# Optimization experiments

Hardware: AMD Instinct MI355X
Metric: run time of the kernel (lower is better)

Reference implementation:

```python
import jax, jax.numpy as jnp
import numpy as np

B, T, D = 4, 2048, 1024

def layer_norm(x, gamma, bias):
    # NOTE: faithfully reproduces the source's (buggy) LN: x - mu/sqrt(var), unbiased var
    mu = jnp.mean(x, axis=-1, keepdims=True)
    var = jnp.var(x, axis=-1, ddof=1, keepdims=True)
    return (x - mu / jnp.sqrt(var)) * gamma + bias

def setup_inputs() -> dict:
    key = jax.random.key(0)
    ks = jax.random.split(key, 8)
    scale = 1.0 / np.sqrt(D)
    return {
        'x': jax.random.normal(ks[0], (B, T, D), dtype=jnp.float32),
        'gamma1': jnp.ones((D,), jnp.float32),
        'beta1': jnp.zeros((D,), jnp.float32),
        'w_q': jax.random.uniform(ks[1], (D, D), jnp.float32, -scale, scale),
        'w_k': jax.random.uniform(ks[2], (D, D), jnp.float32, -scale, scale),
        'w_v': jax.random.uniform(ks[3], (D, D), jnp.float32, -scale, scale),
        'gamma2': jnp.ones((D,), jnp.float32),
        'beta2': jnp.zeros((D,), jnp.float32),
        'W1': jax.random.uniform(ks[4], (D, D), jnp.float32, -scale, scale),
        'b1': jnp.zeros((D,), jnp.float32),
        'W2': jax.random.uniform(ks[5], (D, D), jnp.float32, -scale, scale),
        'b2': jnp.zeros((D,), jnp.float32),
    }

def reference(x, gamma1, beta1, w_q, w_k, w_v, gamma2, beta2, W1, b1, W2, b2):
    d_model = x.shape[-1]
    t = x.shape[1]
    h = layer_norm(x, gamma1, beta1)
    q = jnp.einsum('btk,kd->btd', h, w_q)
    k = jnp.einsum('btk,kd->btd', h, w_k)
    v = jnp.einsum('btk,kd->btd', h, w_v)
    scale = 1.0 / jnp.sqrt(jnp.asarray(d_model, x.dtype))
    causal = jnp.tril(jnp.ones((t, t), dtype=bool))
    mask = jnp.where(causal, 0.0, -jnp.inf).astype(x.dtype)
    scores = jnp.einsum('bqd,bkd->bqk', q, k) * scale + mask
    attn = jax.nn.softmax(scores, axis=-1)
    y = jnp.einsum('bqt,btd->bqd', attn, v) + x
    h2 = layer_norm(y, gamma2, beta2)
    out = jnp.maximum(h2 @ W1 + b1, 0.0) @ W2 + b2
    return out + y
```

## Files before the change

### kernel.cpp

```cpp
#include <hip/hip_runtime.h>
#include <hip/hip_bf16.h>
#include <math.h>

using bf16 = __hip_bfloat16;

static constexpr int Bn = 4;
static constexpr int Tn = 2048;
static constexpr int Dn = 1024;

typedef __attribute__((ext_vector_type(8))) short bf16x8;
typedef __attribute__((ext_vector_type(4))) float f32x4;

__device__ __forceinline__ float ldf(float v) { return v; }
__device__ __forceinline__ float ldf(bf16 v) { return __bfloat162float(v); }
__device__ __forceinline__ bf16 f2b(float v) { return __float2bfloat16(v); }
__device__ __forceinline__ float b2f(short s) {
    return __uint_as_float(((unsigned)(unsigned short)s) << 16);
}
__device__ __forceinline__ short f2bs(float v) {
    bf16 t = __float2bfloat16(v);
    return *reinterpret_cast<short*>(&t);
}

template <typename T> __device__ __forceinline__ T from_float(float v);
template <> __device__ __forceinline__ float from_float<float>(float v) { return v; }
template <> __device__ __forceinline__ bf16 from_float<bf16>(float v) { return f2b(v); }

__device__ __forceinline__ void load4(const float* p, float* v) {
    const float4 t = *(const float4*)p;
    v[0] = t.x; v[1] = t.y; v[2] = t.z; v[3] = t.w;
}
__device__ __forceinline__ void load4(const bf16* p, float* v) {
    const short4 t = *(const short4*)p;
    v[0] = b2f(t.x); v[1] = b2f(t.y); v[2] = b2f(t.z); v[3] = b2f(t.w);
}

__device__ __forceinline__ void async_copy16(const bf16* g, bf16* l) {
    __builtin_amdgcn_global_load_lds(
        (const __attribute__((address_space(1))) void*)g,
        (__attribute__((address_space(3))) void*)l,
        16, 0, 0);
}

template <int BN, int EPI, typename OutT, bool RELU>
__global__ __launch_bounds__(512, 2) void gemm8p(
    const bf16* __restrict__ A, const bf16* __restrict__ Bm,
    OutT* __restrict__ C, const float* __restrict__ bias,
    const bf16* __restrict__ res, bf16* __restrict__ vtp,
    int K, int lda, int ldb, int ldc)
{
    static_assert(EPI != 1 || BN == 128, "V-transpose epilogue needs BN=128");
    constexpr int BM = 256, BK = 32;
    constexpr int NT = BN / 64;
    constexpr int BUFE = (BM + BN) * BK;
    __shared__ __align__(16) bf16 smem[3 * BUFE];

    const int bm = blockIdx.x, bn = blockIdx.y;
    const int tid = threadIdx.x;
    const int wave = tid >> 6;
    const int lane = tid & 63;
    const int wm = wave >> 2;
    const int wn = wave & 3;
    const int lr = lane >> 2;
    const int lc = (lane & 3) * 8;
    const int arow = lane & 15;
    const int kq = (lane >> 4) * 8;

    const int NK = K / BK;

    const bf16* gA0 = A + (size_t)(bm * BM + wave * 16 + lr) * lda + lc;
    const bf16* gA1 = A + (size_t)(bm * BM + (wave + 8) * 16 + lr) * lda + lc;
    const bf16* gB0 = Bm + (size_t)(bn * BN + wave * 16 + lr) * ldb + lc;
    const bf16* gB1 = (BN == 256)
        ? Bm + (size_t)(bn * BN + (wave + 8) * 16 + lr) * ldb + lc : nullptr;

    f32x4 acc[8][NT] = {};

    {
        bf16* As0 = smem;
        bf16* Bs0 = smem + BM * BK;
        bf16* As1 = smem + BUFE;
        bf16* Bs1 = smem + BUFE + BM * BK;
        async_copy16(gA0, As0 + wave * 512);
        async_copy16(gA1, As0 + (wave + 8) * 512);
        async_copy16(gB0, Bs0 + wave * 512);
        if constexpr (BN == 256) async_copy16(gB1, Bs0 + (wave + 8) * 512);
        async_copy16(gA0 + BK, As1 + wave * 512);
        async_copy16(gA1 + BK, As1 + (wave + 8) * 512);
        async_copy16(gB0 + BK, Bs1 + wave * 512);
        if constexpr (BN == 256) async_copy16(gB1 + BK, Bs1 + (wave + 8) * 512);
    }
    if constexpr (BN == 256) asm volatile("s_waitcnt vmcnt(4)" ::: "memory");
    else                     asm volatile("s_waitcnt vmcnt(3)" ::: "memory");
    __builtin_amdgcn_s_barrier();

    int cb = 0;
    int sb = 2;
    for (int kt = 0; kt < NK; ++kt) {
        const bf16* As = smem + cb * BUFE;
        const bf16* Bs = As + BM * BK;
        const bool st = (kt + 2) < NK;
        const int koff = (kt + 2) * BK;

        bf16x8 af[8], bf0[NT / 2];
#pragma unroll
        for (int mt = 0; mt < 8; ++mt)
            af[mt] = *(const bf16x8*)&As[(wm * 8 + mt) * 512 + arow * 32 + kq];
#pragma unroll
        for (int nt = 0; nt < NT / 2; ++nt)
            bf0[nt] = *(const bf16x8*)&Bs[(wn * NT + nt) * 512 + arow * 32 + kq];
        if (st) {
            bf16* Ad = smem + sb * BUFE;
            async_copy16(gA0 + koff, Ad + wave * 512);
            async_copy16(gA1 + koff, Ad + (wave + 8) * 512);
        }
        __builtin_amdgcn_s_barrier();
        asm volatile("s_waitcnt lgkmcnt(0)" ::: "memory");
        __builtin_amdgcn_sched_barrier(0);
        __builtin_amdgcn_s_setprio(1);
#pragma unroll
        for (int mt = 0; mt < 8; ++mt)
#pragma unroll
            for (int nt = 0; nt < NT / 2; ++nt)
                acc[mt][nt] = __builtin_amdgcn_mfma_f32_16x16x32_bf16(
                    af[mt], bf0[nt], acc[mt][nt], 0, 0, 0);
        __builtin_amdgcn_s_setprio(0);
        __builtin_amdgcn_s_barrier();

        bf16x8 bf1[NT / 2];
#pragma unroll
        for (int nt = 0; nt < NT / 2; ++nt)
            bf1[nt] = *(const bf16x8*)&Bs[(wn * NT + NT / 2 + nt) * 512 + arow * 32 + kq];
        if (st) {
            bf16* Bd = smem + sb * BUFE + BM * BK;
            async_copy16(gB0 + koff, Bd + wave * 512);
            if constexpr (BN == 256) async_copy16(gB1 + koff, Bd + (wave + 8) * 512);
        }
        __builtin_amdgcn_s_barrier();
        asm volatile("s_waitcnt lgkmcnt(0)" ::: "memory");
        __builtin_amdgcn_sched_barrier(0);
        __builtin_amdgcn_s_setprio(1);
#pragma unroll
        for (int mt = 0; mt < 8; ++mt)
#pragma unroll
            for (int nt = 0; nt < NT / 2; ++nt)
                acc[mt][NT / 2 + nt] = __builtin_amdgcn_mfma_f32_16x16x32_bf16(
                    af[mt], bf1[nt], acc[mt][NT / 2 + nt], 0, 0, 0);
        __builtin_amdgcn_s_setprio(0);
        if (st) {
            if constexpr (BN == 256) asm volatile("s_waitcnt vmcnt(4)" ::: "memory");
            else                     asm volatile("s_waitcnt vmcnt(3)" ::: "memory");
        } else {
            asm volatile("s_waitcnt vmcnt(0)" ::: "memory");
        }
        __builtin_amdgcn_s_barrier();

        cb = (cb + 1 == 3) ? 0 : cb + 1;
        sb = (sb + 1 == 3) ? 0 : sb + 1;
    }

    const int qrow = (lane >> 4) * 4;
    const int ccol = lane & 15;

    if constexpr (EPI == 1) {
        bf16* tt = smem;
#pragma unroll
        for (int mt = 0; mt < 8; ++mt)
#pragma unroll
            for (int nt = 0; nt < NT; ++nt) {
                const int dl = wn * (NT * 16) + nt * 16 + ccol;
                const int tl = wm * 128 + mt * 16 + qrow;
                short4 o;
                o.x = f2bs(acc[mt][nt][0]);
                o.y = f2bs(acc[mt][nt][1]);
                o.z = f2bs(acc[mt][nt][2]);
                o.w = f2bs(acc[mt][nt][3]);
                *(short4*)&tt[dl * 264 + tl] = o;
            }
        __syncthreads();
        const int b = (bm * BM) >> 11;
        const int tin = (bm * BM) & (Tn - 1);
        const int dr = tid >> 4;
        const int t0 = (tid & 15) * 16;
#pragma unroll
        for (int p = 0; p < 4; ++p) {
            const int d = p * 32 + dr;
            const bf16* srcl = &tt[d * 264 + t0];
            bf16* dst = vtp + ((size_t)b * Dn + bn * BN + d) * Tn + tin + t0;
            ((bf16x8*)dst)[0] = ((const bf16x8*)srcl)[0];
            ((bf16x8*)dst)[1] = ((const bf16x8*)srcl)[1];
        }
        return;
    }

    const int row0 = bm * BM + wm * 128;
    const int col0 = bn * BN + wn * (NT * 16);
#pragma unroll
    for (int mt = 0; mt < 8; ++mt)
#pragma unroll
        for (int nt = 0; nt < NT; ++nt) {
            const int cc = col0 + nt * 16 + ccol;
            const float bv = bias ? bias[cc] : 0.0f;
#pragma unroll
            for (int r = 0; r < 4; ++r) {
                const int rr = row0 + mt * 16 + qrow + r;
                float v = acc[mt][nt][r] + bv;
                if (RELU) v = fmaxf(v, 0.0f);
                if (res) v += b2f(*(const short*)&res[(size_t)rr * ldc + cc]);
                C[(size_t)rr * ldc + cc] = from_float<OutT>(v);
            }
        }
}

template <int BM, int BN, int MINW, int EPI, typename OutT, typename ResT, bool RELU>
__global__ __launch_bounds__(256, MINW) void gemm_nt(
    const bf16* __restrict__ A, const bf16* __restrict__ Bm,
    OutT* __restrict__ C, float* __restrict__ c2,
    const float* __restrict__ bias,
    const ResT* __restrict__ res, float* __restrict__ rowsum,
    int M, int N, int K, int lda, int ldb, int ldc,
    long sA, long sB, long sC, long sR, int mode)
{
    int bm, bn, bz, chunk = 0;
    if (mode == 5) {
        bn = blockIdx.x; bz = blockIdx.y;
        const int zc = blockIdx.z;
        bm = 15 - (zc >> 1);
        chunk = zc & 1;
    } else if (mode == 4) {
        bn = blockIdx.x; bz = blockIdx.y;
        bm = (int)gridDim.z - 1 - (int)blockIdx.z;
    } else {
        bm = blockIdx.x; bn = blockIdx.y; bz = blockIdx.z;
    }
    if (mode == 4 && bn * BN > bm * BM + (BM - 1)) return;

    int kbeg = 0, kmax = K;
    if (mode == 5) {
        const int keff = (bm + 1) * BM;
        const int half = keff >> 1;
        kbeg = chunk ? half : 0;
        kmax = chunk ? keff : half;
    }

    const bf16* Ab = A + (size_t)bz * sA;
    const bf16* Bb = Bm + (size_t)bz * sB;

    constexpr int WROWS = BM / 64;
    constexpr int WCOLS = 4 / WROWS;
    constexpr int TM = 64;
    constexpr int TN = BN / WCOLS;
    constexpr int MT = TM / 16;
    constexpr int NT = TN / 16;
    constexpr int nA = BM / 16;
    constexpr int nB = BN / 16;
    constexpr int STAGE = 2 * (BM + BN) * 32;

    __shared__ __align__(16) bf16 smem[STAGE];
    bf16* As = smem;
    bf16* Bs = smem + 2 * BM * 32;

    const int tid = threadIdx.x;
    const int wave = tid >> 6;
    const int lane = tid & 63;
    const int wm = wave / WCOLS;
    const int wn = wave % WCOLS;

    f32x4 acc[MT][NT] = {};

    const int lr = lane >> 2;
    const int lc = (lane & 3) * 8;
    const bf16* gAc[nA / 4]; bf16* lAc[nA / 4];
    const bf16* gBc[nB / 4]; bf16* lBc[nB / 4];
#pragma unroll
    for (int i = 0; i < nA / 4; ++i) {
        const int c = wave + 4 * i;
        gAc[i] = Ab + (size_t)(bm * BM + c * 16 + lr) * lda + lc;
        lAc[i] = &As[c * 512];
    }
#pragma unroll
    for (int i = 0; i < nB / 4; ++i) {
        const int c = wave + 4 * i;
        gBc[i] = Bb + (size_t)(bn * BN + c * 16 + lr) * ldb + lc;
        lBc[i] = &Bs[c * 512];
    }

    const int arow = lane & 15;
    const int kq = (lane >> 4) * 8;

    for (int k0 = kbeg; k0 < kmax; k0 += 64) {
#pragma unroll
        for (int hh = 0; hh < 2; ++hh) {
#pragma unroll
            for (int i = 0; i < nA / 4; ++i)
                async_copy16(gAc[i] + k0 + 32 * hh, lAc[i] + hh * (BM * 32));
#pragma unroll
            for (int i = 0; i < nB / 4; ++i)
                async_copy16(gBc[i] + k0 + 32 * hh, lBc[i] + hh * (BN * 32));
        }
        __syncthreads();

#pragma unroll
        for (int hh = 0; hh < 2; ++hh) {
            const bf16* Ah = As + hh * (BM * 32);
            const bf16* Bh = Bs + hh * (BN * 32);
            bf16x8 af[MT], bfm[NT];
#pragma unroll
            for (int t = 0; t < MT; ++t)
                af[t] = *(const bf16x8*)&Ah[(wm * TM + t * 16 + arow) * 32 + kq];
#pragma unroll
            for (int t = 0; t < NT; ++t)
                bfm[t] = *(const bf16x8*)&Bh[(wn * TN + t * 16 + arow) * 32 + kq];
#pragma unroll
            for (int mt = 0; mt < MT; ++mt)
#pragma unroll
                for (int nt = 0; nt < NT; ++nt)
                    acc[mt][nt] = __builtin_amdgcn_mfma_f32_16x16x32_bf16(
                        af[mt], bfm[nt], acc[mt][nt], 0, 0, 0);
        }
        __syncthreads();
    }

    const int rowBase = bm * BM + wm * TM;
    const int colBase = bn * BN + wn * TN;
    const int qrow = (lane >> 4) * 4;
    const int ccol = lane & 15;

    if (EPI == 2) {
        OutT* Cb = C + (size_t)bz * sC;
        float* rsb = rowsum + (size_t)bz * Tn;
        const float scale = 0.03125f;
#pragma unroll
        for (int mt = 0; mt < MT; ++mt) {
            float rsv[4] = {0.f, 0.f, 0.f, 0.f};
#pragma unroll
            for (int nt = 0; nt < NT; ++nt) {
                const int cc = colBase + nt * 16 + ccol;
#pragma unroll
                for (int r = 0; r < 4; ++r) {
                    const int rr = rowBase + mt * 16 + qrow + r;
                    float e = 0.0f;
                    if (cc <= rr) {
                        const short es = f2bs(__expf(acc[mt][nt][r] * scale));
                        Cb[(size_t)rr * ldc + cc] = *(const bf16*)&es;
                        e = b2f(es);
                    } else {
                        Cb[(size_t)rr * ldc + cc] = from_float<OutT>(0.0f);
                    }
                    rsv[r] += e;
                }
            }
#pragma unroll
            for (int r = 0; r < 4; ++r) {
                float v = rsv[r];
                v += __shfl_xor(v, 1);
                v += __shfl_xor(v, 2);
                v += __shfl_xor(v, 4);
                v += __shfl_xor(v, 8);
                if (ccol == 0)
                    atomicAdd(rsb + rowBase + mt * 16 + qrow + r, v);
            }
        }
        return;
    }

    OutT* Cb = C + (size_t)bz * sC;
    if (mode == 5 && chunk) Cb = (OutT*)(c2 + (size_t)bz * sC);
    const ResT* Rb = res ? (res + (size_t)bz * sR) : nullptr;
#pragma unroll
    for (int mt = 0; mt < MT; ++mt) {
#pragma unroll
        for (int nt = 0; nt < NT; ++nt) {
            const int cc = colBase + nt * 16 + ccol;
            const float bv = bias ? bias[cc] : 0.0f;
#pragma unroll
            for (int r = 0; r < 4; ++r) {
                const int rr = rowBase + mt * 16 + qrow + r;
                float v = acc[mt][nt][r] + bv;
                if (RELU) v = fmaxf(v, 0.0f);
                if (Rb) v += ldf(Rb[(size_t)rr * ldc + cc]);
                Cb[(size_t)rr * ldc + cc] = from_float<OutT>(v);
            }
        }
    }
}

template <typename InT>
__device__ __forceinline__ void ln_row(
    const InT* __restrict__ xr, const float* __restrict__ gamma,
    const float* __restrict__ beta, bf16* __restrict__ orow, int tid)
{
    const int j = tid * 4;
    float v[4];
    load4(xr + j, v);
    float s = v[0] + v[1] + v[2] + v[3];
    float sq = v[0] * v[0] + v[1] * v[1] + v[2] * v[2] + v[3] * v[3];
#pragma unroll
    for (int o = 32; o > 0; o >>= 1) {
        s += __shfl_down(s, o);
        sq += __shfl_down(sq, o);
    }
    __shared__ float red[2][4];
    const int lane = tid & 63, w = tid >> 6;
    if (lane == 0) { red[0][w] = s; red[1][w] = sq; }
    __syncthreads();
    s  = red[0][0] + red[0][1] + red[0][2] + red[0][3];
    sq = red[1][0] + red[1][1] + red[1][2] + red[1][3];
    const float mean = s / (float)Dn;
    const float var = (sq - s * s / (float)Dn) / (float)(Dn - 1);
    const float coef = mean * rsqrtf(var);

    const float4 g = *(const float4*)(gamma + j);
    const float4 be = *(const float4*)(beta + j);
    short4 o;
    o.x = f2bs((v[0] - coef) * g.x + be.x);
    o.y = f2bs((v[1] - coef) * g.y + be.y);
    o.z = f2bs((v[2] - coef) * g.z + be.z);
    o.w = f2bs((v[3] - coef) * g.w + be.w);
    *(short4*)(orow + j) = o;
}

__global__ __launch_bounds__(256) void ln2_fused(
    const float* __restrict__ yp0, const float* __restrict__ yp1,
    const float* __restrict__ rowsum, const float* __restrict__ x,
    const float* __restrict__ gamma, const float* __restrict__ beta,
    bf16* __restrict__ y, bf16* __restrict__ h2)
{
    const int row = blockIdx.x;
    const int tid = threadIdx.x;
    const int j = tid * 4;
    const size_t base = (size_t)row * Dn;
    const float inv = 1.0f / rowsum[row];

    float p0[4], p1[4], xv[4], v[4];
    load4(yp0 + base + j, p0);
    load4(yp1 + base + j, p1);
    load4(x + base + j, xv);
    short4 yo;
    v[0] = (p0[0] + p1[0]) * inv + xv[0];
    v[1] = (p0[1] + p1[1]) * inv + xv[1];
    v[2] = (p0[2] + p1[2]) * inv + xv[2];
    v[3] = (p0[3] + p1[3]) * inv + xv[3];
    yo.x = f2bs(v[0]); yo.y = f2bs(v[1]); yo.z = f2bs(v[2]); yo.w = f2bs(v[3]);
    *(short4*)(y + base + j) = yo;

    float s = v[0] + v[1] + v[2] + v[3];
    float sq = v[0] * v[0] + v[1] * v[1] + v[2] * v[2] + v[3] * v[3];
#pragma unroll
    for (int o = 32; o > 0; o >>= 1) {
        s += __shfl_down(s, o);
        sq += __shfl_down(sq, o);
    }
    __shared__ float red[2][4];
    const int lane = tid & 63, w = tid >> 6;
    if (lane == 0) { red[0][w] = s; red[1][w] = sq; }
    __syncthreads();
    s  = red[0][0] + red[0][1] + red[0][2] + red[0][3];
    sq = red[1][0] + red[1][1] + red[1][2] + red[1][3];
    const float mean = s / (float)Dn;
    const float var = (sq - s * s / (float)Dn) / (float)(Dn - 1);
    const float coef = mean * rsqrtf(var);

    const float4 g = *(const float4*)(gamma + j);
    const float4 be = *(const float4*)(beta + j);
    short4 o;
    o.x = f2bs((v[0] - coef) * g.x + be.x);
    o.y = f2bs((v[1] - coef) * g.y + be.y);
    o.z = f2bs((v[2] - coef) * g.z + be.z);
    o.w = f2bs((v[3] - coef) * g.w + be.w);
    *(short4*)(h2 + base + j) = o;
}

struct WPtrs { const float* p[5]; };

__global__ __launch_bounds__(256) void prep_kernel(
    WPtrs wp, bf16* __restrict__ wdst, float* __restrict__ rowsum,
    const float* __restrict__ x, const float* __restrict__ gamma1,
    const float* __restrict__ beta1, bf16* __restrict__ h)
{
    const int bx = blockIdx.x;
    if (bx < 5120) {
        __shared__ bf16 tile[32][33];
        const int z = bx >> 10;
        const int t = bx & 1023;
        const float* src = wp.p[z];
        bf16* d = wdst + (size_t)z * Dn * Dn;
        const int c0 = (t & 31) * 32, r0 = (t >> 5) * 32;
        const int tx = threadIdx.x & 31;
        const int ty = threadIdx.x >> 5;
#pragma unroll
        for (int dy = 0; dy < 32; dy += 8)
            tile[ty + dy][tx] = f2b(src[(size_t)(r0 + ty + dy) * Dn + (c0 + tx)]);
        __syncthreads();
#pragma unroll
        for (int dy = 0; dy < 32; dy += 8)
            d[(size_t)(c0 + ty + dy) * Dn + (r0 + tx)] = tile[tx][ty + dy];
    } else if (bx < 5128) {
        const int base = (bx - 5120) * 1024;
#pragma unroll
        for (int i = 0; i < 4; ++i) rowsum[base + i * 256 + threadIdx.x] = 0.0f;
    } else {
        const int row = bx - 5128;
        ln_row(x + (size_t)row * Dn, gamma1, beta1, h + (size_t)row * Dn, threadIdx.x);
    }
}

extern "C" void kernel_launch(void* const* d_in, const int* in_sizes, int n_in,
                              void* d_out, int out_size, void* d_ws, size_t ws_size,
                              hipStream_t stream) {
    const float* x      = (const float*)d_in[0];
    const float* gamma1 = (const float*)d_in[1];
    const float* beta1  = (const float*)d_in[2];
    const float* w_q    = (const float*)d_in[3];
    const float* w_k    = (const float*)d_in[4];
    const float* w_v    = (const float*)d_in[5];
    const float* gamma2 = (const float*)d_in[6];
    const float* beta2  = (const float*)d_in[7];
    const float* W1     = (const float*)d_in[8];
    const float* b1     = (const float*)d_in[9];
    const float* W2     = (const float*)d_in[10];
    const float* b2     = (const float*)d_in[11];
    float* out = (float*)d_out;

    char* ws = (char*)d_ws;
    size_t off = 0;
    auto alloc = [&](size_t bytes) {
        char* p = ws + off;
        off += (bytes + 255) & ~(size_t)255;
        return p;
    };
    const size_t BT = (size_t)Bn * Tn;
    bf16* h    = (bf16*)alloc(BT * Dn * 2);
    bf16* qk   = (bf16*)alloc(BT * 2 * Dn * 2);
    bf16* vt   = (bf16*)alloc(BT * Dn * 2);
    bf16* wbuf = (bf16*)alloc((size_t)5 * Dn * Dn * 2);
    bf16* S    = (bf16*)alloc((size_t)Bn * Tn * Tn * 2);
    bf16* y    = (bf16*)alloc(BT * Dn * 2);
    float* rowsum = (float*)alloc((size_t)Bn * Tn * 4);
    float* yp1 = (float*)alloc(BT * Dn * 4);
    float* yp0 = (float*)qk;
    bf16* h2   = h;
    bf16* mid  = qk;

    const dim3 blk(256);
    const dim3 blk512(512);
    const long TD  = (long)Tn * Dn;
    const long TT  = (long)Tn * Tn;
    const long TD2 = (long)Tn * 2 * Dn;
    const size_t DD = (size_t)Dn * Dn;

    WPtrs wp; wp.p[0] = w_q; wp.p[1] = w_k; wp.p[2] = w_v; wp.p[3] = W1; wp.p[4] = W2;
    prep_kernel<<<dim3(5128 + (unsigned)BT, 1, 1), blk, 0, stream>>>(
        wp, wbuf, rowsum, x, gamma1, beta1, h);

    gemm8p<256, 0, bf16, false><<<dim3(32, 8, 1), blk512, 0, stream>>>(
        h, wbuf, qk, nullptr, nullptr, nullptr, Dn, Dn, Dn, 2 * Dn);

    gemm8p<128, 1, bf16, false><<<dim3(32, 8, 1), blk512, 0, stream>>>(
        h, wbuf + 2 * DD, (bf16*)nullptr, nullptr, nullptr, vt,
        Dn, Dn, Dn, 0);

    gemm_nt<128, 128, 4, 2, bf16, float, false><<<dim3(16, Bn, 16), blk, 0, stream>>>(
        qk, qk + 1024, S, nullptr, nullptr, nullptr, rowsum,
        Tn, Tn, Dn, 2 * Dn, 2 * Dn, Tn, TD2, TD2, TT, 0, 4);

    gemm_nt<128, 128, 4, 0, float, float, false><<<dim3(8, Bn, 32), blk, 0, stream>>>(
        S, vt, yp0, yp1, nullptr, nullptr, nullptr,
        Tn, Dn, Tn, Tn, Tn, Dn, TT, TD, TD, 0, 5);

    ln2_fused<<<dim3((unsigned)BT), blk, 0, stream>>>(
        yp0, yp1, rowsum, x, gamma2, beta2, y, h2);

    gemm_nt<128, 128, 4, 0, bf16, float, true><<<dim3(64, 8, 1), blk, 0, stream>>>(
        h2, wbuf + 3 * DD, mid, nullptr, b1, nullptr, nullptr,
        (int)BT, Dn, Dn, Dn, Dn, Dn, 0, 0, 0, 0, 0);

    gemm_nt<128, 128, 4, 0, float, bf16, false><<<dim3(64, 8, 1), blk, 0, stream>>>(
        mid, wbuf + 4 * DD, out, nullptr, b2, y, nullptr,
        (int)BT, Dn, Dn, Dn, Dn, Dn, 0, 0, 0, 0, 0);
}
```

Before: 352.4 us.

## Move causal QK^T and PV attention GEMMs onto 256-tile triple-buffered gemm8p kernel

```diff
diff --git a/kernel.cpp b/kernel.cpp
--- a/kernel.cpp
+++ b/kernel.cpp
@@ -42,12 +42,13 @@
         16, 0, 0);
 }
 
-template <int BN, int EPI, typename OutT, bool RELU>
+template <int BN, int EPI, int MODE, typename OutT>
 __global__ __launch_bounds__(512, 2) void gemm8p(
     const bf16* __restrict__ A, const bf16* __restrict__ Bm,
-    OutT* __restrict__ C, const float* __restrict__ bias,
-    const bf16* __restrict__ res, bf16* __restrict__ vtp,
-    int K, int lda, int ldb, int ldc)
+    OutT* __restrict__ C, float* __restrict__ c2,
+    const float* __restrict__ bias, const bf16* __restrict__ res,
+    bf16* __restrict__ vtp, float* __restrict__ rowsum,
+    int K, int lda, int ldb, int ldc, long sA, long sB, long sC)
 {
     static_assert(EPI != 1 || BN == 128, "V-transpose epilogue needs BN=128");
     constexpr int BM = 256, BK = 32;
@@ -55,7 +56,31 @@
     constexpr int BUFE = (BM + BN) * BK;
     __shared__ __align__(16) bf16 smem[3 * BUFE];
 
-    const int bm = blockIdx.x, bn = blockIdx.y;
+    int bm, bn, bz = 0, chunk = 0;
+    if constexpr (MODE == 1) {
+        bn = blockIdx.x; bz = blockIdx.y; bm = blockIdx.z;
+        if (bn > bm) return;
+    } else if constexpr (MODE == 2) {
+        bn = blockIdx.x; bz = blockIdx.y;
+        const int zc = blockIdx.z;
+        bm = 7 - (zc >> 1);
+        chunk = zc & 1;
+    } else {
+        bm = blockIdx.x; bn = blockIdx.y; bz = blockIdx.z;
+    }
+
+    int kbeg = 0, kmax = K;
+    if constexpr (MODE == 2) {
+        const int keff = (bm + 1) * BM;
+        const int half = keff >> 1;
+        kbeg = chunk ? half : 0;
+        kmax = chunk ? keff : half;
+    }
+    const int NK = (kmax - kbeg) >> 5;
+
+    const bf16* Ab = A + (size_t)bz * sA;
+    const bf16* Bb = Bm + (size_t)bz * sB;
+
     const int tid = threadIdx.x;
     const int wave = tid >> 6;
     const int lane = tid & 63;
@@ -66,13 +91,11 @@
     const int arow = lane & 15;
     const int kq = (lane >> 4) * 8;
 
-    const int NK = K / BK;
-
-    const bf16* gA0 = A + (size_t)(bm * BM + wave * 16 + lr) * lda + lc;
-    const bf16* gA1 = A + (size_t)(bm * BM + (wave + 8) * 16 + lr) * lda + lc;
-    const bf16* gB0 = Bm + (size_t)(bn * BN + wave * 16 + lr) * ldb + lc;
+    const bf16* gA0 = Ab + (size_t)(bm * BM + wave * 16 + lr) * lda + lc + kbeg;
+    const bf16* gA1 = Ab + (size_t)(bm * BM + (wave + 8) * 16 + lr) * lda + lc + kbeg;
+    const bf16* gB0 = Bb + (size_t)(bn * BN + wave * 16 + lr) * ldb + lc + kbeg;
     const bf16* gB1 = (BN == 256)
-        ? Bm + (size_t)(bn * BN + (wave + 8) * 16 + lr) * ldb + lc : nullptr;
+        ? Bb + (size_t)(bn * BN + (wave + 8) * 16 + lr) * ldb + lc + kbeg : nullptr;
 
     f32x4 acc[8][NT] = {};
 
@@ -161,6 +184,8 @@
 
     const int qrow = (lane >> 4) * 4;
     const int ccol = lane & 15;
+    const int row0 = bm * BM + wm * 128;
+    const int col0 = bn * BN + wn * (NT * 16);
 
     if constexpr (EPI == 1) {
         bf16* tt = smem;
@@ -193,152 +218,19 @@
         return;
     }
 
-    const int row0 = bm * BM + wm * 128;
-    const int col0 = bn * BN + wn * (NT * 16);
-#pragma unroll
-    for (int mt = 0; mt < 8; ++mt)
-#pragma unroll
-        for (int nt = 0; nt < NT; ++nt) {
-            const int cc = col0 + nt * 16 + ccol;
-            const float bv = bias ? bias[cc] : 0.0f;
-#pragma unroll
-            for (int r = 0; r < 4; ++r) {
-                const int rr = row0 + mt * 16 + qrow + r;
-                float v = acc[mt][nt][r] + bv;
-                if (RELU) v = fmaxf(v, 0.0f);
-                if (res) v += b2f(*(const short*)&res[(size_t)rr * ldc + cc]);
-                C[(size_t)rr * ldc + cc] = from_float<OutT>(v);
-            }
-        }
-}
-
-template <int BM, int BN, int MINW, int EPI, typename OutT, typename ResT, bool RELU>
-__global__ __launch_bounds__(256, MINW) void gemm_nt(
-    const bf16* __restrict__ A, const bf16* __restrict__ Bm,
-    OutT* __restrict__ C, float* __restrict__ c2,
-    const float* __restrict__ bias,
-    const ResT* __restrict__ res, float* __restrict__ rowsum,
-    int M, int N, int K, int lda, int ldb, int ldc,
-    long sA, long sB, long sC, long sR, int mode)
-{
-    int bm, bn, bz, chunk = 0;
-    if (mode == 5) {
-        bn = blockIdx.x; bz = blockIdx.y;
-        const int zc = blockIdx.z;
-        bm = 15 - (zc >> 1);
-        chunk = zc & 1;
-    } else if (mode == 4) {
-        bn = blockIdx.x; bz = blockIdx.y;
-        bm = (int)gridDim.z - 1 - (int)blockIdx.z;
-    } else {
-        bm = blockIdx.x; bn = blockIdx.y; bz = blockIdx.z;
-    }
-    if (mode == 4 && bn * BN > bm * BM + (BM - 1)) return;
-
-    int kbeg = 0, kmax = K;
-    if (mode == 5) {
-        const int keff = (bm + 1) * BM;
-        const int half = keff >> 1;
-        kbeg = chunk ? half : 0;
-        kmax = chunk ? keff : half;
-    }
-
-    const bf16* Ab = A + (size_t)bz * sA;
-    const bf16* Bb = Bm + (size_t)bz * sB;
-
-    constexpr int WROWS = BM / 64;
-    constexpr int WCOLS = 4 / WROWS;
-    constexpr int TM = 64;
-    constexpr int TN = BN / WCOLS;
-    constexpr int MT = TM / 16;
-    constexpr int NT = TN / 16;
-    constexpr int nA = BM / 16;
-    constexpr int nB = BN / 16;
-    constexpr int STAGE = 2 * (BM + BN) * 32;
-
-    __shared__ __align__(16) bf16 smem[STAGE];
-    bf16* As = smem;
-    bf16* Bs = smem + 2 * BM * 32;
-
-    const int tid = threadIdx.x;
-    const int wave = tid >> 6;
-    const int lane = tid & 63;
-    const int wm = wave / WCOLS;
-    const int wn = wave % WCOLS;
-
-    f32x4 acc[MT][NT] = {};
-
-    const int lr = lane >> 2;
-    const int lc = (lane & 3) * 8;
-    const bf16* gAc[nA / 4]; bf16* lAc[nA / 4];
-    const bf16* gBc[nB / 4]; bf16* lBc[nB / 4];
-#pragma unroll
-    for (int i = 0; i < nA / 4; ++i) {
-        const int c = wave + 4 * i;
-        gAc[i] = Ab + (size_t)(bm * BM + c * 16 + lr) * lda + lc;
-        lAc[i] = &As[c * 512];
-    }
-#pragma unroll
-    for (int i = 0; i < nB / 4; ++i) {
-        const int c = wave + 4 * i;
-        gBc[i] = Bb + (size_t)(bn * BN + c * 16 + lr) * ldb + lc;
-        lBc[i] = &Bs[c * 512];
-    }
-
-    const int arow = lane & 15;
-    const int kq = (lane >> 4) * 8;
-
-    for (int k0 = kbeg; k0 < kmax; k0 += 64) {
-#pragma unroll
-        for (int hh = 0; hh < 2; ++hh) {
-#pragma unroll
-            for (int i = 0; i < nA / 4; ++i)
-                async_copy16(gAc[i] + k0 + 32 * hh, lAc[i] + hh * (BM * 32));
-#pragma unroll
-            for (int i = 0; i < nB / 4; ++i)
-                async_copy16(gBc[i] + k0 + 32 * hh, lBc[i] + hh * (BN * 32));
-        }
-        __syncthreads();
-
-#pragma unroll
-        for (int hh = 0; hh < 2; ++hh) {
-            const bf16* Ah = As + hh * (BM * 32);
-            const bf16* Bh = Bs + hh * (BN * 32);
-            bf16x8 af[MT], bfm[NT];
-#pragma unroll
-            for (int t = 0; t < MT; ++t)
-                af[t] = *(const bf16x8*)&Ah[(wm * TM + t * 16 + arow) * 32 + kq];
-#pragma unroll
-            for (int t = 0; t < NT; ++t)
-                bfm[t] = *(const bf16x8*)&Bh[(wn * TN + t * 16 + arow) * 32 + kq];
-#pragma unroll
-            for (int mt = 0; mt < MT; ++mt)
-#pragma unroll
-                for (int nt = 0; nt < NT; ++nt)
-                    acc[mt][nt] = __builtin_amdgcn_mfma_f32_16x16x32_bf16(
-                        af[mt], bfm[nt], acc[mt][nt], 0, 0, 0);
-        }
-        __syncthreads();
-    }
-
-    const int rowBase = bm * BM + wm * TM;
-    const int colBase = bn * BN + wn * TN;
-    const int qrow = (lane >> 4) * 4;
-    const int ccol = lane & 15;
-
-    if (EPI == 2) {
+    if constexpr (EPI == 2) {
         OutT* Cb = C + (size_t)bz * sC;
         float* rsb = rowsum + (size_t)bz * Tn;
         const float scale = 0.03125f;
 #pragma unroll
-        for (int mt = 0; mt < MT; ++mt) {
+        for (int mt = 0; mt < 8; ++mt) {
             float rsv[4] = {0.f, 0.f, 0.f, 0.f};
 #pragma unroll
             for (int nt = 0; nt < NT; ++nt) {
-                const int cc = colBase + nt * 16 + ccol;
+                const int cc = col0 + nt * 16 + ccol;
 #pragma unroll
                 for (int r = 0; r < 4; ++r) {
-                    const int rr = rowBase + mt * 16 + qrow + r;
+                    const int rr = row0 + mt * 16 + qrow + r;
                     float e = 0.0f;
                     if (cc <= rr) {
                         const short es = f2bs(__expf(acc[mt][nt][r] * scale));
@@ -358,15 +250,133 @@
                 v += __shfl_xor(v, 4);
                 v += __shfl_xor(v, 8);
                 if (ccol == 0)
-                    atomicAdd(rsb + rowBase + mt * 16 + qrow + r, v);
+                    atomicAdd(rsb + row0 + mt * 16 + qrow + r, v);
             }
         }
         return;
     }
 
-    OutT* Cb = C + (size_t)bz * sC;
-    if (mode == 5 && chunk) Cb = (OutT*)(c2 + (size_t)bz * sC);
-    const ResT* Rb = res ? (res + (size_t)bz * sR) : nullptr;
+    if constexpr (EPI == 3) {
+        float* Cb = (chunk ? c2 : (float*)C) + (size_t)bz * sC;
+#pragma unroll
+        for (int mt = 0; mt < 8; ++mt)
+#pragma unroll
+            for (int nt = 0; nt < NT; ++nt) {
+                const int cc = col0 + nt * 16 + ccol;
+#pragma unroll
+                for (int r = 0; r < 4; ++r) {
+                    const int rr = row0 + mt * 16 + qrow + r;
+                    Cb[(size_t)rr * ldc + cc] = acc[mt][nt][r];
+                }
+            }
+        return;
+    }
+
+#pragma unroll
+    for (int mt = 0; mt < 8; ++mt)
+#pragma unroll
+        for (int nt = 0; nt < NT; ++nt) {
+            const int cc = col0 + nt * 16 + ccol;
+            const float bv = bias ? bias[cc] : 0.0f;
+#pragma unroll
+            for (int r = 0; r < 4; ++r) {
+                const int rr = row0 + mt * 16 + qrow + r;
+                float v = acc[mt][nt][r] + bv;
+                if (res) v += b2f(*(const short*)&res[(size_t)rr * ldc + cc]);
+                C[(size_t)rr * ldc + cc] = from_float<OutT>(v);
+            }
+        }
+}
+
+template <int BM, int BN, int MINW, int EPI, typename OutT, typename ResT, bool RELU>
+__global__ __launch_bounds__(256, MINW) void gemm_nt(
+    const bf16* __restrict__ A, const bf16* __restrict__ Bm,
+    OutT* __restrict__ C, const float* __restrict__ bias,
+    const ResT* __restrict__ res,
+    int M, int N, int K, int lda, int ldb, int ldc)
+{
+    const int bm = blockIdx.x, bn = blockIdx.y;
+
+    constexpr int WROWS = BM / 64;
+    constexpr int WCOLS = 4 / WROWS;
+    constexpr int TM = 64;
+    constexpr int TN = BN / WCOLS;
+    constexpr int MT = TM / 16;
+    constexpr int NT = TN / 16;
+    constexpr int nA = BM / 16;
+    constexpr int nB = BN / 16;
+    constexpr int STAGE = 2 * (BM + BN) * 32;
+
+    __shared__ __align__(16) bf16 smem[STAGE];
+    bf16* As = smem;
+    bf16* Bs = smem + 2 * BM * 32;
+
+    const int tid = threadIdx.x;
+    const int wave = tid >> 6;
+    const int lane = tid & 63;
+    const int wm = wave / WCOLS;
+    const int wn = wave % WCOLS;
+
+    f32x4 acc[MT][NT] = {};
+
+    const int lr = lane >> 2;
+    const int lc = (lane & 3) * 8;
+    const bf16* gAc[nA / 4]; bf16* lAc[nA / 4];
+    const bf16* gBc[nB / 4]; bf16* lBc[nB / 4];
+#pragma unroll
+    for (int i = 0; i < nA / 4; ++i) {
+        const int c = wave + 4 * i;
+        gAc[i] = A + (size_t)(bm * BM + c * 16 + lr) * lda + lc;
+        lAc[i] = &As[c * 512];
+    }
+#pragma unroll
+    for (int i = 0; i < nB / 4; ++i) {
+        const int c = wave + 4 * i;
+        gBc[i] = Bm + (size_t)(bn * BN + c * 16 + lr) * ldb + lc;
+        lBc[i] = &Bs[c * 512];
+    }
+
+    const int arow = lane & 15;
+    const int kq = (lane >> 4) * 8;
+
+    for (int k0 = 0; k0 < K; k0 += 64) {
+#pragma unroll
+        for (int hh = 0; hh < 2; ++hh) {
+#pragma unroll
+            for (int i = 0; i < nA / 4; ++i)
+                async_copy16(gAc[i] + k0 + 32 * hh, lAc[i] + hh * (BM * 32));
+#pragma unroll
+            for (int i = 0; i < nB / 4; ++i)
+                async_copy16(gBc[i] + k0 + 32 * hh, lBc[i] + hh * (BN * 32));
+        }
+        __syncthreads();
+
+#pragma unroll
+        for (int hh = 0; hh < 2; ++hh) {
+            const bf16* Ah = As + hh * (BM * 32);
+            const bf16* Bh = Bs + hh * (BN * 32);
+            bf16x8 af[MT], bfm[NT];
+#pragma unroll
+            for (int t = 0; t < MT; ++t)
+                af[t] = *(const bf16x8*)&Ah[(wm * TM + t * 16 + arow) * 32 + kq];
+#pragma unroll
+            for (int t = 0; t < NT; ++t)
+                bfm[t] = *(const bf16x8*)&Bh[(wn * TN + t * 16 + arow) * 32 + kq];
+#pragma unroll
+            for (int mt = 0; mt < MT; ++mt)
+#pragma unroll
+                for (int nt = 0; nt < NT; ++nt)
+                    acc[mt][nt] = __builtin_amdgcn_mfma_f32_16x16x32_bf16(
+                        af[mt], bfm[nt], acc[mt][nt], 0, 0, 0);
+        }
+        __syncthreads();
+    }
+
+    const int rowBase = bm * BM + wm * TM;
+    const int colBase = bn * BN + wn * TN;
+    const int qrow = (lane >> 4) * 4;
+    const int ccol = lane & 15;
+
 #pragma unroll
     for (int mt = 0; mt < MT; ++mt) {
 #pragma unroll
@@ -378,8 +388,8 @@
                 const int rr = rowBase + mt * 16 + qrow + r;
                 float v = acc[mt][nt][r] + bv;
                 if (RELU) v = fmaxf(v, 0.0f);
-                if (Rb) v += ldf(Rb[(size_t)rr * ldc + cc]);
-                Cb[(size_t)rr * ldc + cc] = from_float<OutT>(v);
+                if (res) v += ldf(res[(size_t)rr * ldc + cc]);
+                C[(size_t)rr * ldc + cc] = from_float<OutT>(v);
             }
         }
     }
@@ -553,29 +563,30 @@
     prep_kernel<<<dim3(5128 + (unsigned)BT, 1, 1), blk, 0, stream>>>(
         wp, wbuf, rowsum, x, gamma1, beta1, h);
 
-    gemm8p<256, 0, bf16, false><<<dim3(32, 8, 1), blk512, 0, stream>>>(
-        h, wbuf, qk, nullptr, nullptr, nullptr, Dn, Dn, Dn, 2 * Dn);
-
-    gemm8p<128, 1, bf16, false><<<dim3(32, 8, 1), blk512, 0, stream>>>(
-        h, wbuf + 2 * DD, (bf16*)nullptr, nullptr, nullptr, vt,
-        Dn, Dn, Dn, 0);
-
-    gemm_nt<128, 128, 4, 2, bf16, float, false><<<dim3(16, Bn, 16), blk, 0, stream>>>(
-        qk, qk + 1024, S, nullptr, nullptr, nullptr, rowsum,
-        Tn, Tn, Dn, 2 * Dn, 2 * Dn, Tn, TD2, TD2, TT, 0, 4);
-
-    gemm_nt<128, 128, 4, 0, float, float, false><<<dim3(8, Bn, 32), blk, 0, stream>>>(
-        S, vt, yp0, yp1, nullptr, nullptr, nullptr,
-        Tn, Dn, Tn, Tn, Tn, Dn, TT, TD, TD, 0, 5);
+    gemm8p<256, 0, 0, bf16><<<dim3(32, 8, 1), blk512, 0, stream>>>(
+        h, wbuf, qk, nullptr, nullptr, nullptr, nullptr, nullptr,
+        Dn, Dn, Dn, 2 * Dn, 0, 0, 0);
+
+    gemm8p<128, 1, 0, bf16><<<dim3(32, 8, 1), blk512, 0, stream>>>(
+        h, wbuf + 2 * DD, (bf16*)nullptr, nullptr, nullptr, nullptr, vt, nullptr,
+        Dn, Dn, Dn, 0, 0, 0, 0);
+
+    gemm8p<256, 2, 1, bf16><<<dim3(8, Bn, 8), blk512, 0, stream>>>(
+        qk, qk + 1024, S, nullptr, nullptr, nullptr, nullptr, rowsum,
+        Dn, 2 * Dn, 2 * Dn, Tn, TD2, TD2, TT);
+
+    gemm8p<256, 3, 2, float><<<dim3(4, Bn, 16), blk512, 0, stream>>>(
+        S, vt, yp0, yp1, nullptr, nullptr, nullptr, nullptr,
+        Tn, Tn, Tn, Dn, TT, TD, TD);
 
     ln2_fused<<<dim3((unsigned)BT), blk, 0, stream>>>(
         yp0, yp1, rowsum, x, gamma2, beta2, y, h2);
 
     gemm_nt<128, 128, 4, 0, bf16, float, true><<<dim3(64, 8, 1), blk, 0, stream>>>(
-        h2, wbuf + 3 * DD, mid, nullptr, b1, nullptr, nullptr,
-        (int)BT, Dn, Dn, Dn, Dn, Dn, 0, 0, 0, 0, 0);
+        h2, wbuf + 3 * DD, mid, b1, nullptr,
+        (int)BT, Dn, Dn, Dn, Dn, Dn);
 
     gemm_nt<128, 128, 4, 0, float, bf16, false><<<dim3(64, 8, 1), blk, 0, stream>>>(
-        mid, wbuf + 4 * DD, out, nullptr, b2, y, nullptr,
-        (int)BT, Dn, Dn, Dn, Dn, Dn, 0, 0, 0, 0, 0);
-}
+        mid, wbuf + 4 * DD, out, b2, y,
+        (int)BT, Dn, Dn, Dn, Dn, Dn);
+}
```

Result: no change. 352.5 us (+0.0%).
